# Kernel optimization log

Hardware: AMD Instinct MI355X
Metric: run time of the kernel (lower is better)

## Reference

```python
import jax, jax.numpy as jnp
import numpy as np

B, T, D = 2048, 200, 128


def setup_inputs() -> dict:
    key = jax.random.key(0)
    ks = jax.random.split(key, 6)
    query = jax.random.normal(ks[0], (B, D), dtype=jnp.float32)
    keys = jax.random.normal(ks[1], (B, T, D), dtype=jnp.float32)
    mask = jax.random.randint(ks[2], (B, T), 0, 2).astype(jnp.bool_)
    # nn.Linear(4D, D): weight [D, 4D], bias [D]
    lim1 = 1.0 / np.sqrt(4 * D)
    w1 = jax.random.uniform(ks[3], (D, 4 * D), minval=-lim1, maxval=lim1, dtype=jnp.float32)
    b1 = jnp.zeros((D,), dtype=jnp.float32)
    # PReLU single learnable slope (torch default init 0.25)
    prelu_a = jnp.asarray(0.25, dtype=jnp.float32)
    # nn.Linear(D, 1): weight [1, D] stored here as [D, 1], bias scalar
    lim2 = 1.0 / np.sqrt(D)
    w2 = jax.random.uniform(ks[4], (D, 1), minval=-lim2, maxval=lim2, dtype=jnp.float32)
    b2 = jnp.zeros((1,), dtype=jnp.float32)
    return {"query": query, "keys": keys, "mask": mask,
            "w1": w1, "b1": b1, "prelu_a": prelu_a, "w2": w2, "b2": b2}


def reference(query, keys, mask, w1, b1, prelu_a, w2, b2):
    # query: [B, D], keys: [B, T, D], mask: [B, T] bool
    q = jnp.broadcast_to(query[:, None, :], keys.shape)           # [B, T, D]
    x = jnp.concatenate([q, keys, q - keys, q * keys], axis=-1)   # [B, T, 4D]
    h = jnp.einsum('btf,df->btd', x, w1) + b1                     # [B, T, D]
    h = jnp.where(h >= 0, h, prelu_a * h)                         # PReLU
    scores = (h @ w2)[..., 0] + b2[0]                             # [B, T]
    scores = jnp.where(mask, scores, jnp.asarray(-1e9, scores.dtype))
    w = jax.nn.softmax(scores, axis=-1) * mask.astype(scores.dtype)
    w = w / jnp.maximum(w.sum(axis=-1, keepdims=True), 1e-6)
    return jnp.einsum('bt,btd->bd', w, keys)                      # [B, D]
```

## Files before the change

kernel.cpp:

```cpp
#include <hip/hip_runtime.h>
#include <hip/hip_bf16.h>

namespace {

constexpr int T  = 200;
constexpr int D  = 128;
constexpr int NT = 13;

typedef float f32x4 __attribute__((ext_vector_type(4)));
typedef short bf16x8 __attribute__((ext_vector_type(8)));
typedef unsigned int u32;
typedef u32 u32x4 __attribute__((ext_vector_type(4)));

__device__ __forceinline__ short f2bf(float f) {
  __hip_bfloat16 h = __float2bfloat16(f);
  return __builtin_bit_cast(short, h);
}
__device__ __forceinline__ float bflo2f(u32 u) { return __uint_as_float(u << 16); }
__device__ __forceinline__ float bfhi2f(u32 u) { return __uint_as_float(u & 0xFFFF0000u); }

template <int CTRL>
__device__ __forceinline__ float dpp_add(float x) {
  int y = __builtin_amdgcn_update_dpp(0, __float_as_int(x), CTRL, 0xF, 0xF, true);
  return x + __int_as_float(y);
}
__device__ __forceinline__ float sum16(float x) {
  x = dpp_add<0x121>(x);
  x = dpp_add<0x122>(x);
  x = dpp_add<0x124>(x);
  x = dpp_add<0x128>(x);
  return x;
}

constexpr int OFF_U2   = 8192;
constexpr int OFF_OUTL = 8448;
constexpr int OFF_RED  = 8960;
constexpr int SMEM_F   = 8968;

__global__ void pre_kernel(const float* __restrict__ w1, u32* __restrict__ MD,
                           float* __restrict__ sT) {
  int idx = blockIdx.x * 256 + threadIdx.x;
  int d = idx >> 7, f = idx & 127;
  const float* r = w1 + (size_t)d * 512;
  u32 lo = (unsigned short)f2bf(r[128 + f] - r[256 + f]);
  u32 hi = (unsigned short)f2bf(r[384 + f]);
  MD[idx] = lo | (hi << 16);
  sT[(size_t)f * 128 + d] = r[f] + r[256 + f];
}

__global__ __launch_bounds__(256, 2) void din_kernel(
    const float* __restrict__ qg, const float* __restrict__ keysg,
    const void* __restrict__ maskg, const float* __restrict__ w1g,
    const float* __restrict__ b1g, const float* __restrict__ pag,
    const float* __restrict__ w2g, const float* __restrict__ b2g,
    const u32* __restrict__ MD, const float* __restrict__ sT,
    int usePre, float* __restrict__ outg) {
  __shared__ __align__(16) float smem[SMEM_F];
  float* u2   = smem + OFF_U2;
  float* outl = smem + OFF_OUTL;
  float* red  = smem + OFF_RED;

  const int tid  = threadIdx.x;
  const int b    = blockIdx.x;
  const int wid  = tid >> 6;
  const int lane = tid & 63;
  const int lrow = (lane >> 4) & 3;
  const int lcol = lane & 15;

  const float* qb    = qg + (size_t)b * D;
  const float* keysB = keysg + (size_t)b * T * D;

  int mcode;
  {
    unsigned v = ((const unsigned*)maskg)[lane];
    unsigned c0 = v & 255u, c1 = (v >> 8) & 255u, c2 = (v >> 16) & 255u, c3 = v >> 24;
    bool weird = (c0 == 0x80u) | (c0 == 0x3Fu) | (c1 == 0x80u) | (c1 == 0x3Fu) |
                 (c2 == 0x80u) | (c2 == 0x3Fu) | (c3 == 0x80u) | (c3 == 0x3Fu);
    bool nz = (v & 0xFFFFFF00u) != 0u;
    unsigned long long bw = __ballot(weird);
    unsigned long long bn = __ballot(nz);
    mcode = bw ? 2 : (bn ? 1 : 0);
  }

  const float pa  = pag[0];
  const float b2v = b2g[0];

  f32x4 ka0[4], ka1[4], kb0[4], kb1[4];
  #define LOADK(K0, K1, TILE)                                        \
    do {                                                             \
      int trow_ = (TILE) * 16 + lcol;                                \
      int trc_  = trow_ < T ? trow_ : T - 1;                         \
      const float* kr_ = keysB + (size_t)trc_ * D + lrow * 8;        \
      _Pragma("unroll")                                              \
      for (int ks = 0; ks < 4; ++ks) {                               \
        K0[ks] = *(const f32x4*)(kr_ + ks * 32);                     \
        K1[ks] = *(const f32x4*)(kr_ + ks * 32 + 4);                 \
      }                                                              \
    } while (0)

  LOADK(ka0, ka1, wid);
  LOADK(kb0, kb1, wid + 4);

  if (usePre) {
    #pragma unroll
    for (int i = 0; i < 8; ++i) {
      int e = i * 2048 + tid * 8;
      int d = e >> 7, f = e & 127;
      u32x4 A = *(const u32x4*)(MD + e);
      u32x4 B = *(const u32x4*)(MD + e + 4);
      f32x4 q0 = *(const f32x4*)(qb + f), q1 = *(const f32x4*)(qb + f + 4);
      bf16x8 v;
      v[0] = f2bf(bflo2f(A.x) + bfhi2f(A.x) * q0.x);
      v[1] = f2bf(bflo2f(A.y) + bfhi2f(A.y) * q0.y);
      v[2] = f2bf(bflo2f(A.z) + bfhi2f(A.z) * q0.z);
      v[3] = f2bf(bflo2f(A.w) + bfhi2f(A.w) * q0.w);
      v[4] = f2bf(bflo2f(B.x) + bfhi2f(B.x) * q1.x);
      v[5] = f2bf(bflo2f(B.y) + bfhi2f(B.y) * q1.y);
      v[6] = f2bf(bflo2f(B.z) + bfhi2f(B.z) * q1.z);
      v[7] = f2bf(bflo2f(B.w) + bfhi2f(B.w) * q1.w);
      int slot = (f >> 3) ^ (d & 15);
      *(bf16x8*)((char*)smem + d * 256 + slot * 16) = v;
    }
  } else {
    #pragma unroll
    for (int i = 0; i < 8; ++i) {
      int e = i * 2048 + tid * 8;
      int d = e >> 7, f = e & 127;
      const float* r = w1g + (size_t)d * 512;
      f32x4 bB0 = *(const f32x4*)(r + 128 + f), bB1 = *(const f32x4*)(r + 128 + f + 4);
      f32x4 cC0 = *(const f32x4*)(r + 256 + f), cC1 = *(const f32x4*)(r + 256 + f + 4);
      f32x4 dd0 = *(const f32x4*)(r + 384 + f), dd1 = *(const f32x4*)(r + 384 + f + 4);
      f32x4 q0 = *(const f32x4*)(qb + f), q1 = *(const f32x4*)(qb + f + 4);
      bf16x8 v;
      v[0] = f2bf(bB0.x - cC0.x + dd0.x * q0.x);
      v[1] = f2bf(bB0.y - cC0.y + dd0.y * q0.y);
      v[2] = f2bf(bB0.z - cC0.z + dd0.z * q0.z);
      v[3] = f2bf(bB0.w - cC0.w + dd0.w * q0.w);
      v[4] = f2bf(bB1.x - cC1.x + dd1.x * q1.x);
      v[5] = f2bf(bB1.y - cC1.y + dd1.y * q1.y);
      v[6] = f2bf(bB1.z - cC1.z + dd1.z * q1.z);
      v[7] = f2bf(bB1.w - cC1.w + dd1.w * q1.w);
      int slot = (f >> 3) ^ (d & 15);
      *(bf16x8*)((char*)smem + d * 256 + slot * 16) = v;
    }
  }

  {
    int d = tid & 127, fh = tid >> 7;
    float acc = 0.f;
    if (usePre) {
      const float* sp = sT + (size_t)(fh * 64) * 128 + d;
      const float* qh = qb + fh * 64;
      #pragma unroll
      for (int i = 0; i < 64; ++i) acc += qh[i] * sp[(size_t)i * 128];
    } else {
      const float* arow = w1g + (size_t)d * 512 + fh * 64;
      const float* crow = arow + 256;
      const float* qh   = qb + fh * 64;
      #pragma unroll
      for (int i = 0; i < 16; ++i) {
        f32x4 qv = *(const f32x4*)(qh + i * 4);
        f32x4 av = *(const f32x4*)(arow + i * 4);
        f32x4 cv = *(const f32x4*)(crow + i * 4);
        acc += qv.x * (av.x + cv.x) + qv.y * (av.y + cv.y) +
               qv.z * (av.z + cv.z) + qv.w * (av.w + cv.w);
      }
    }
    if (fh == 0) acc += b1g[d];
    u2[fh * 128 + d] = acc;
  }

  __syncthreads();

  float m_w = -1e9f, den_w = 0.f;
  float accpv[32];
  #pragma unroll
  for (int i = 0; i < 32; ++i) accpv[i] = 0.f;

  #define COMPUTE(TILE, K0, K1)                                              \
    do {                                                                     \
      const int tile_ = (TILE);                                              \
      bf16x8 af[4];                                                          \
      _Pragma("unroll")                                                      \
      for (int ks = 0; ks < 4; ++ks) {                                       \
        af[ks][0] = f2bf(K0[ks].x); af[ks][1] = f2bf(K0[ks].y);              \
        af[ks][2] = f2bf(K0[ks].z); af[ks][3] = f2bf(K0[ks].w);              \
        af[ks][4] = f2bf(K1[ks].x); af[ks][5] = f2bf(K1[ks].y);              \
        af[ks][6] = f2bf(K1[ks].z); af[ks][7] = f2bf(K1[ks].w);              \
      }                                                                      \
      float sj[4] = {0.f, 0.f, 0.f, 0.f};                                    \
      _Pragma("unroll")                                                      \
      for (int dt = 0; dt < 8; ++dt) {                                       \
        int d_ = dt * 16 + lcol;                                             \
        f32x4 acc = {0.f, 0.f, 0.f, 0.f};                                    \
        _Pragma("unroll")                                                    \
        for (int ks = 0; ks < 4; ++ks) {                                     \
          bf16x8 bfv = *(const bf16x8*)((const char*)smem + d_ * 256 +       \
                                        (((ks * 4 + lrow) ^ (d_ & 15)) << 4)); \
          acc = __builtin_amdgcn_mfma_f32_16x16x32_bf16(af[ks], bfv, acc, 0, 0, 0); \
        }                                                                    \
        float u_d = u2[d_] + u2[128 + d_];                                   \
        float w2d = w2g[d_];                                                 \
        _Pragma("unroll")                                                    \
        for (int j = 0; j < 4; ++j) {                                        \
          float h = acc[j] + u_d;                                            \
          h = (h >= 0.f) ? h : pa * h;                                       \
          sj[j] += h * w2d;                                                  \
        }                                                                    \
      }                                                                      \
      _Pragma("unroll")                                                      \
      for (int j = 0; j < 4; ++j) sj[j] = sum16(sj[j]);                      \
      float mt = -1e30f;                                                     \
      _Pragma("unroll")                                                      \
      for (int j = 0; j < 4; ++j) {                                          \
        int t_ = tile_ * 16 + lrow * 4 + j;                                  \
        bool valid = (t_ < T);                                               \
        if (valid) {                                                         \
          size_t mi = (size_t)b * T + t_;                                    \
          if (mcode == 0)      valid = ((const int*)maskg)[mi] != 0;         \
          else if (mcode == 1) valid = ((const unsigned char*)maskg)[mi] != 0; \
          else                 valid = ((const float*)maskg)[mi] != 0.f;     \
        }                                                                    \
        sj[j] = valid ? (sj[j] + b2v) : -1e30f;                              \
        mt = fmaxf(mt, sj[j]);                                               \
      }                                                                      \
      mt = fmaxf(mt, __shfl_xor(mt, 16));                                    \
      mt = fmaxf(mt, __shfl_xor(mt, 32));                                    \
      if (mt > m_w) {                                   \
        float sc = __expf(m_w - mt);                                         \
        den_w *= sc;                                                         \
        _Pragma("unroll")                                                    \
        for (int i = 0; i < 32; ++i) accpv[i] *= sc;                         \
        m_w = mt;                                                            \
      }                                                                      \
      float wj[4], dsum = 0.f;                                               \
      _Pragma("unroll")                                                      \
      for (int j = 0; j < 4; ++j) { wj[j] = __expf(sj[j] - m_w); dsum += wj[j]; } \
      dsum += __shfl_xor(dsum, 16);                                          \
      dsum += __shfl_xor(dsum, 32);                                          \
      den_w += dsum;                                                         \
      float tmp = (lcol & 2) ? ((lcol & 1) ? wj[3] : wj[2])                  \
                             : ((lcol & 1) ? wj[1] : wj[0]);                 \
      float wtr = __shfl(tmp, ((lcol >> 2) << 4) | (lcol & 3), 64);          \
      _Pragma("unroll")                                                      \
      for (int ks = 0; ks < 4; ++ks) {                                       \
        accpv[ks * 8 + 0] += wtr * K0[ks].x;                                 \
        accpv[ks * 8 + 1] += wtr * K0[ks].y;                                 \
        accpv[ks * 8 + 2] += wtr * K0[ks].z;                                 \
        accpv[ks * 8 + 3] += wtr * K0[ks].w;                                 \
        accpv[ks * 8 + 4] += wtr * K1[ks].x;                                 \
        accpv[ks * 8 + 5] += wtr * K1[ks].y;                                 \
        accpv[ks * 8 + 6] += wtr * K1[ks].z;                                 \
        accpv[ks * 8 + 7] += wtr * K1[ks].w;                                 \
      }                                                                      \
    } while (0)

  COMPUTE(wid, ka0, ka1);
  LOADK(ka0, ka1, wid + 8);
  COMPUTE(wid + 4, kb0, kb1);
  if (wid == 0) LOADK(kb0, kb1, 12);
  COMPUTE(wid + 8, ka0, ka1);
  if (wid == 0) COMPUTE(12, kb0, kb1);

  #pragma unroll
  for (int i = 0; i < 32; ++i) accpv[i] = sum16(accpv[i]);
  if (lcol == 0) {
    #pragma unroll
    for (int ks = 0; ks < 4; ++ks) {
      f32x4 a = {accpv[ks * 8 + 0], accpv[ks * 8 + 1], accpv[ks * 8 + 2], accpv[ks * 8 + 3]};
      f32x4 c = {accpv[ks * 8 + 4], accpv[ks * 8 + 5], accpv[ks * 8 + 6], accpv[ks * 8 + 7]};
      *(f32x4*)(outl + wid * 128 + ks * 32 + lrow * 8)     = a;
      *(f32x4*)(outl + wid * 128 + ks * 32 + lrow * 8 + 4) = c;
    }
  }
  if (lane == 0) { red[wid] = m_w; red[4 + wid] = den_w; }

  __syncthreads();

  if (tid < 128) {
    float M = fmaxf(fmaxf(red[0], red[1]), fmaxf(red[2], red[3]));
    float den = 0.f, o = 0.f;
    #pragma unroll
    for (int w = 0; w < 4; ++w) {
      float scw = __expf(red[w] - M);
      den += red[4 + w] * scw;
      o   += outl[w * 128 + tid] * scw;
    }
    float inv = (den > 0.f) ? 1.0f / den : 0.f;
    outg[(size_t)b * D + tid] = o * inv;
  }
  #undef COMPUTE
  #undef LOADK
}

}

extern "C" void kernel_launch(void* const* d_in, const int* in_sizes, int n_in,
                              void* d_out, int out_size, void* d_ws, size_t ws_size,
                              hipStream_t stream) {
  (void)in_sizes; (void)n_in; (void)out_size;
  const float* q    = (const float*)d_in[0];
  const float* keys = (const float*)d_in[1];
  const void*  mask = d_in[2];
  const float* w1   = (const float*)d_in[3];
  const float* b1   = (const float*)d_in[4];
  const float* pa   = (const float*)d_in[5];
  const float* w2   = (const float*)d_in[6];
  const float* b2   = (const float*)d_in[7];
  float* out = (float*)d_out;

  u32* MD   = (u32*)d_ws;
  float* sT = (float*)((char*)d_ws + 65536);
  int usePre = (ws_size >= (size_t)131072) ? 1 : 0;
  if (usePre) pre_kernel<<<64, 256, 0, stream>>>(w1, MD, sT);
  din_kernel<<<2048, 256, 0, stream>>>(q, keys, mask, w1, b1, pa, w2, b2,
                                       MD, sT, usePre, out);
}
```

Measured before the change: 88.76 us.

## Precompute per-batch query projection in separate kernel, ballot-pack mask, cache w2

Adds a preU kernel that computes the per-batch query projection u = q·(W_a+W_c)+b1 into workspace, so the main kernel only loads 128 floats instead of doing a strided 64-element dot per thread. The mask is read once up front with coalesced loads and packed into 64-bit ballot words, replacing per-tile scattered mask loads. w2 values are cached in registers, and s_setprio is raised around the MFMA loop. The cost is an extra kernel launch and a round trip of the u vectors through global memory. When the workspace is too small, the kernel falls back to the old paths.

New measurement: 75.43 us. -15.0%, faster.

```diff
diff --git a/kernel.cpp b/kernel.cpp
--- a/kernel.cpp
+++ b/kernel.cpp
@@ -4,7 +4,6 @@
 namespace {
 
 constexpr int T  = 200;
-constexpr int D  = 128;
 constexpr int NT = 13;
 
 typedef float f32x4 __attribute__((ext_vector_type(4)));
@@ -25,10 +24,8 @@
   return x + __int_as_float(y);
 }
 __device__ __forceinline__ float sum16(float x) {
-  x = dpp_add<0x121>(x);
-  x = dpp_add<0x122>(x);
-  x = dpp_add<0x124>(x);
-  x = dpp_add<0x128>(x);
+  x = dpp_add<0x121>(x); x = dpp_add<0x122>(x);
+  x = dpp_add<0x124>(x); x = dpp_add<0x128>(x);
   return x;
 }
 
@@ -38,14 +35,32 @@
 constexpr int SMEM_F   = 8968;
 
 __global__ void pre_kernel(const float* __restrict__ w1, u32* __restrict__ MD,
-                           float* __restrict__ sT) {
+                           float* __restrict__ sTf) {
   int idx = blockIdx.x * 256 + threadIdx.x;
   int d = idx >> 7, f = idx & 127;
   const float* r = w1 + (size_t)d * 512;
   u32 lo = (unsigned short)f2bf(r[128 + f] - r[256 + f]);
   u32 hi = (unsigned short)f2bf(r[384 + f]);
   MD[idx] = lo | (hi << 16);
-  sT[(size_t)f * 128 + d] = r[f] + r[256 + f];
+  sTf[(size_t)f * 128 + d] = r[f] + r[256 + f];
+}
+
+__global__ void preU_kernel(const float* __restrict__ qg, const float* __restrict__ sTf,
+                            const float* __restrict__ b1g, float* __restrict__ uall) {
+  __shared__ float qs[128];
+  int b = blockIdx.x, d = threadIdx.x;
+  qs[d] = qg[(size_t)b * 128 + d];
+  __syncthreads();
+  float acc = b1g[d];
+  #pragma unroll 16
+  for (int f = 0; f < 128; ++f) acc += qs[f] * sTf[(size_t)f * 128 + d];
+  uall[(size_t)b * 128 + d] = acc;
+}
+
+__device__ __forceinline__ bool mask_at(const void* m, int mcode, size_t i) {
+  if (mcode == 0) return ((const int*)m)[i] != 0;
+  if (mcode == 1) return ((const unsigned char*)m)[i] != 0;
+  return ((const float*)m)[i] != 0.f;
 }
 
 __global__ __launch_bounds__(256, 2) void din_kernel(
@@ -53,8 +68,8 @@
     const void* __restrict__ maskg, const float* __restrict__ w1g,
     const float* __restrict__ b1g, const float* __restrict__ pag,
     const float* __restrict__ w2g, const float* __restrict__ b2g,
-    const u32* __restrict__ MD, const float* __restrict__ sT,
-    int usePre, float* __restrict__ outg) {
+    const u32* __restrict__ MD, const float* __restrict__ uall,
+    int mode, float* __restrict__ outg) {
   __shared__ __align__(16) float smem[SMEM_F];
   float* u2   = smem + OFF_U2;
   float* outl = smem + OFF_OUTL;
@@ -67,8 +82,8 @@
   const int lrow = (lane >> 4) & 3;
   const int lcol = lane & 15;
 
-  const float* qb    = qg + (size_t)b * D;
-  const float* keysB = keysg + (size_t)b * T * D;
+  const float* qb    = qg + (size_t)b * 128;
+  const float* keysB = keysg + (size_t)b * T * 128;
 
   int mcode;
   {
@@ -90,7 +105,7 @@
     do {                                                             \
       int trow_ = (TILE) * 16 + lcol;                                \
       int trc_  = trow_ < T ? trow_ : T - 1;                         \
-      const float* kr_ = keysB + (size_t)trc_ * D + lrow * 8;        \
+      const float* kr_ = keysB + (size_t)trc_ * 128 + lrow * 8;      \
       _Pragma("unroll")                                              \
       for (int ks = 0; ks < 4; ++ks) {                               \
         K0[ks] = *(const f32x4*)(kr_ + ks * 32);                     \
@@ -101,7 +116,17 @@
   LOADK(ka0, ka1, wid);
   LOADK(kb0, kb1, wid + 4);
 
-  if (usePre) {
+  unsigned long long mw0, mw1, mw2, mw3;
+  {
+    size_t base = (size_t)b * T;
+    bool v0 = mask_at(maskg, mcode, base + lane);
+    bool v1 = mask_at(maskg, mcode, base + 64 + lane);
+    bool v2 = mask_at(maskg, mcode, base + 128 + lane);
+    bool v3 = (192 + lane < T) ? mask_at(maskg, mcode, base + 192 + lane) : false;
+    mw0 = __ballot(v0); mw1 = __ballot(v1); mw2 = __ballot(v2); mw3 = __ballot(v3);
+  }
+
+  if (mode >= 1) {
     #pragma unroll
     for (int i = 0; i < 8; ++i) {
       int e = i * 2048 + tid * 8;
@@ -145,32 +170,32 @@
     }
   }
 
-  {
+  if (mode == 2) {
+    if (tid < 128) u2[tid] = uall[(size_t)b * 128 + tid];
+    else if (tid < 256) u2[tid] = 0.f;
+  } else {
     int d = tid & 127, fh = tid >> 7;
+    const float* arow = w1g + (size_t)d * 512 + fh * 64;
+    const float* crow = arow + 256;
+    const float* qh   = qb + fh * 64;
     float acc = 0.f;
-    if (usePre) {
-      const float* sp = sT + (size_t)(fh * 64) * 128 + d;
-      const float* qh = qb + fh * 64;
-      #pragma unroll
-      for (int i = 0; i < 64; ++i) acc += qh[i] * sp[(size_t)i * 128];
-    } else {
-      const float* arow = w1g + (size_t)d * 512 + fh * 64;
-      const float* crow = arow + 256;
-      const float* qh   = qb + fh * 64;
-      #pragma unroll
-      for (int i = 0; i < 16; ++i) {
-        f32x4 qv = *(const f32x4*)(qh + i * 4);
-        f32x4 av = *(const f32x4*)(arow + i * 4);
-        f32x4 cv = *(const f32x4*)(crow + i * 4);
-        acc += qv.x * (av.x + cv.x) + qv.y * (av.y + cv.y) +
-               qv.z * (av.z + cv.z) + qv.w * (av.w + cv.w);
-      }
+    #pragma unroll
+    for (int i = 0; i < 16; ++i) {
+      f32x4 qv = *(const f32x4*)(qh + i * 4);
+      f32x4 av = *(const f32x4*)(arow + i * 4);
+      f32x4 cv = *(const f32x4*)(crow + i * 4);
+      acc += qv.x * (av.x + cv.x) + qv.y * (av.y + cv.y) +
+             qv.z * (av.z + cv.z) + qv.w * (av.w + cv.w);
     }
     if (fh == 0) acc += b1g[d];
     u2[fh * 128 + d] = acc;
   }
 
   __syncthreads();
+
+  float w2w[8];
+  #pragma unroll
+  for (int dt = 0; dt < 8; ++dt) w2w[dt] = w2g[dt * 16 + lcol];
 
   float m_w = -1e9f, den_w = 0.f;
   float accpv[32];
@@ -189,6 +214,7 @@
         af[ks][6] = f2bf(K1[ks].z); af[ks][7] = f2bf(K1[ks].w);              \
       }                                                                      \
       float sj[4] = {0.f, 0.f, 0.f, 0.f};                                    \
+      __builtin_amdgcn_s_setprio(1);                                         \
       _Pragma("unroll")                                                      \
       for (int dt = 0; dt < 8; ++dt) {                                       \
         int d_ = dt * 16 + lcol;                                             \
@@ -200,7 +226,7 @@
           acc = __builtin_amdgcn_mfma_f32_16x16x32_bf16(af[ks], bfv, acc, 0, 0, 0); \
         }                                                                    \
         float u_d = u2[d_] + u2[128 + d_];                                   \
-        float w2d = w2g[d_];                                                 \
+        float w2d = w2w[dt];                                                 \
         _Pragma("unroll")                                                    \
         for (int j = 0; j < 4; ++j) {                                        \
           float h = acc[j] + u_d;                                            \
@@ -208,19 +234,16 @@
           sj[j] += h * w2d;                                                  \
         }                                                                    \
       }                                                                      \
+      __builtin_amdgcn_s_setprio(0);                                         \
       _Pragma("unroll")                                                      \
       for (int j = 0; j < 4; ++j) sj[j] = sum16(sj[j]);                      \
+      unsigned long long mword = tile_ < 4 ? mw0 : tile_ < 8 ? mw1           \
+                                 : tile_ < 12 ? mw2 : mw3;                   \
       float mt = -1e30f;                                                     \
       _Pragma("unroll")                                                      \
       for (int j = 0; j < 4; ++j) {                                          \
-        int t_ = tile_ * 16 + lrow * 4 + j;                                  \
-        bool valid = (t_ < T);                                               \
-        if (valid) {                                                         \
-          size_t mi = (size_t)b * T + t_;                                    \
-          if (mcode == 0)      valid = ((const int*)maskg)[mi] != 0;         \
-          else if (mcode == 1) valid = ((const unsigned char*)maskg)[mi] != 0; \
-          else                 valid = ((const float*)maskg)[mi] != 0.f;     \
-        }                                                                    \
+        int bitp = ((tile_ & 3) << 4) + lrow * 4 + j;                        \
+        bool valid = (mword >> bitp) & 1ull;                                 \
         sj[j] = valid ? (sj[j] + b2v) : -1e30f;                              \
         mt = fmaxf(mt, sj[j]);                                               \
       }                                                                      \
@@ -287,7 +310,7 @@
       o   += outl[w * 128 + tid] * scw;
     }
     float inv = (den > 0.f) ? 1.0f / den : 0.f;
-    outg[(size_t)b * D + tid] = o * inv;
+    outg[(size_t)b * 128 + tid] = o * inv;
   }
   #undef COMPUTE
   #undef LOADK
@@ -309,10 +332,15 @@
   const float* b2   = (const float*)d_in[7];
   float* out = (float*)d_out;
 
-  u32* MD   = (u32*)d_ws;
-  float* sT = (float*)((char*)d_ws + 65536);
-  int usePre = (ws_size >= (size_t)131072) ? 1 : 0;
-  if (usePre) pre_kernel<<<64, 256, 0, stream>>>(w1, MD, sT);
+  u32* MD     = (u32*)d_ws;
+  float* sTf  = (float*)((char*)d_ws + 65536);
+  float* uall = (float*)((char*)d_ws + 131072);
+  int mode = 0;
+  if (ws_size >= (size_t)131072 + (size_t)2048 * 128 * 4) mode = 2;
+  else if (ws_size >= (size_t)131072)                     mode = 1;
+
+  if (mode >= 1) pre_kernel<<<64, 256, 0, stream>>>(w1, MD, sTf);
+  if (mode == 2) preU_kernel<<<2048, 128, 0, stream>>>(q, sTf, b1, uall);
   din_kernel<<<2048, 256, 0, stream>>>(q, keys, mask, w1, b1, pa, w2, b2,
-                                       MD, sT, usePre, out);
-}
+                                       MD, uall, mode, out);
+}
```
